# Optimization experiments

Measured on AMD Instinct MI355X. Metric: run time of the kernel, lower is better.

Reference implementation:

```python
import jax, jax.numpy as jnp
import numpy as np

STRIDES = (8, 16, 32)
IMG = 640
REG_MAX = 16
TOPK = 10
ALPHA = 0.5
BETA = 6.0
EPS_IOU = 1e-16


def _make_anchors():
    # anchor centers for all pyramid levels, (N, 2) in pixel coords
    pts = []
    for s in STRIDES:
        h = w = IMG // s
        ys, xs = jnp.meshgrid(jnp.arange(h, dtype=jnp.float32),
                              jnp.arange(w, dtype=jnp.float32), indexing='ij')
        a = (jnp.stack([xs, ys], axis=-1).reshape(-1, 2) + 0.5) * s
        pts.append(a)
    return jnp.concatenate(pts, axis=0)  # (8400, 2)


def _iou_pairwise(pred, gt):
    # pred (B,N,4), gt (B,M,4) -> IoU (B,M,N)
    b1 = pred[:, None, :, :]   # (B,1,N,4)
    b2 = gt[:, :, None, :]     # (B,M,1,4)
    tl = jnp.maximum(b1[..., :2], b2[..., :2])
    br = jnp.minimum(b1[..., 2:], b2[..., 2:])
    wh = jnp.clip(br - tl, 0.0)
    inter = wh[..., 0] * wh[..., 1]
    a1 = (b1[..., 2] - b1[..., 0]) * (b1[..., 3] - b1[..., 1])
    a2 = (b2[..., 2] - b2[..., 0]) * (b2[..., 3] - b2[..., 1])
    return inter / (a1 + a2 - inter + EPS_IOU)


def _iou_1v1(b1, b2):
    # elementwise IoU, both (..., 4)
    tl = jnp.maximum(b1[..., :2], b2[..., :2])
    br = jnp.minimum(b1[..., 2:], b2[..., 2:])
    wh = jnp.clip(br - tl, 0.0)
    inter = wh[..., 0] * wh[..., 1]
    a1 = (b1[..., 2] - b1[..., 0]) * (b1[..., 3] - b1[..., 1])
    a2 = (b2[..., 2] - b2[..., 0]) * (b2[..., 3] - b2[..., 1])
    return inter / (a1 + a2 - inter + EPS_IOU)


def setup_inputs() -> dict:
    key = jax.random.key(0)
    ks = jax.random.split(key, 6)
    B, N, NC, M = 32, 8400, 80, 40
    pred_scores = jax.random.normal(ks[0], (B, N, NC), jnp.float32)
    pred_dist = jax.random.normal(ks[1], (B, N, 4 * REG_MAX), jnp.float32)
    gt_labels = jax.random.randint(ks[2], (B, M, 1), 0, NC, dtype=jnp.int32)
    cxy = jax.random.uniform(ks[3], (B, M, 2), jnp.float32) * 560.0 + 40.0
    wh = jax.random.uniform(ks[4], (B, M, 2), jnp.float32) * 120.0 + 20.0
    gt_bboxes = jnp.concatenate([jnp.clip(cxy - wh / 2, 0.0, float(IMG)),
                                 jnp.clip(cxy + wh / 2, 0.0, float(IMG))], axis=-1)
    dfl_weight = jax.random.normal(ks[5], (REG_MAX,), jnp.float32) * 0.05
    return {"pred_scores": pred_scores, "pred_dist": pred_dist,
            "gt_labels": gt_labels, "gt_bboxes": gt_bboxes,
            "dfl_weight": dfl_weight}


def reference(pred_scores, pred_dist, gt_labels, gt_bboxes, dfl_weight):
    B, N, NC = pred_scores.shape
    M = gt_bboxes.shape[1]
    anchors = _make_anchors()  # (N, 2)

    # DFL: softmax over reg bins, weighted sum with (random-init) conv weight
    prob = jax.nn.softmax(pred_dist.reshape(B, N, 4, REG_MAX), axis=-1)
    ltrb = prob @ dfl_weight                      # (B,N,4)
    pred_bboxes = jnp.concatenate([anchors - ltrb[..., :2],
                                   anchors + ltrb[..., 2:]], axis=-1)  # (B,N,4) xyxy

    # ---- task-aligned assigner (no-grad) ----
    sg = jax.lax.stop_gradient
    sig = jax.nn.sigmoid(sg(pred_scores))         # (B,N,NC)
    labels = gt_labels[..., 0].astype(jnp.int32)  # (B,M)
    sigT = jnp.swapaxes(sig, 1, 2)                # (B,NC,N)
    scores = jnp.take_along_axis(sigT, jnp.broadcast_to(labels[:, :, None], (B, M, N)), axis=1)  # (B,M,N)
    ious = jnp.clip(_iou_pairwise(sg(pred_bboxes), gt_bboxes), 0.0)      # (B,M,N)
    align = scores ** ALPHA * ious ** BETA        # (B,M,N)

    _, topk_idxs = jax.lax.top_k(align, TOPK)     # (B,M,TOPK) over anchors
    mask = jnp.zeros((B * M, N), dtype=align.dtype)
    mask = mask.at[jnp.arange(B * M)[:, None], topk_idxs.reshape(B * M, TOPK)].set(1.0)
    mask = mask.reshape(B, M, N)
    mask = mask * (align > 1e-9).astype(align.dtype)
    max_m = align.max(axis=1)                     # (B,N) best metric per anchor
    mask = mask * (align == max_m[:, None, :]).astype(align.dtype)

    fg_mask = mask.max(axis=1)                    # (B,N) in {0,1}
    tgt_idx = mask.argmax(axis=1)                 # (B,N) assigned gt index
    ts_sum = jnp.maximum(fg_mask.sum(), 1.0)

    # ---- classification targets (vectorized scatter) ----
    asg_labels = jnp.take_along_axis(labels, tgt_idx, axis=1)  # (B,N)
    target_scores = jax.nn.one_hot(asg_labels, NC, dtype=pred_scores.dtype) * (max_m * fg_mask)[..., None]

    x = pred_scores
    bce = jnp.maximum(x, 0.0) - x * target_scores + jnp.log1p(jnp.exp(-jnp.abs(x)))
    loss_cls = bce.sum() / ts_sum

    # ---- box IoU loss on positives (vectorized gather + mask) ----
    gt_asg = jnp.take_along_axis(gt_bboxes, tgt_idx[..., None], axis=1)  # (B,N,4)
    iou1 = _iou_1v1(pred_bboxes, gt_asg)          # (B,N)
    fg = fg_mask.sum()
    loss_box = jnp.where(fg > 0, ((1.0 - iou1) * fg_mask).sum() / fg, 0.0)

    return loss_cls + loss_box * 1.5
```

## Files before the change

### kernel.cpp

```cpp
#include <hip/hip_runtime.h>
#include <cstdint>
#include <cstddef>

#define BB 32
#define NN 8400
#define NCC 80
#define MM 40
#define RM 16
#define TOPKK 10
#define CAP 2048
#define SLOTP 41
#define AB 64

__device__ __forceinline__ void anchor_xy(int n, float& ax, float& ay) {
    int s, x, y;
    if (n < 6400)      { s = 8;  y = n / 80;            x = n - y * 80; }
    else if (n < 8000) { int i = n - 6400; s = 16; y = i / 40; x = i - y * 40; }
    else               { int i = n - 8000; s = 32; y = i / 20; x = i - y * 20; }
    ax = ((float)x + 0.5f) * (float)s;
    ay = ((float)y + 0.5f) * (float)s;
}

__global__ __launch_bounds__(256) void k_dfl(const float* __restrict__ pd,
                                             const float* __restrict__ w,
                                             float* __restrict__ pbb,
                                             int*   __restrict__ tgt) {
    const int b  = blockIdx.y;
    const int n0 = blockIdx.x * 128;
    const int t  = threadIdx.x;

    if (t < 128 && n0 + t < NN) tgt[(size_t)b * NN + n0 + t] = 0x7F7F7F7F;

    #pragma unroll
    for (int h = 0; h < 2; h++) {
        int f = t + h * 256;
        int a = f >> 2, side = f & 3;
        int n = n0 + a;
        int nc = min(n, NN - 1);
        const float* p = pd + (((size_t)(b * NN + nc)) * 4 + side) * RM;
        float x[RM];
        #pragma unroll
        for (int i = 0; i < 4; i++) {
            float4 v = *(const float4*)(p + i * 4);
            x[i*4+0] = v.x; x[i*4+1] = v.y; x[i*4+2] = v.z; x[i*4+3] = v.w;
        }
        float mx = x[0];
        #pragma unroll
        for (int i = 1; i < RM; i++) mx = fmaxf(mx, x[i]);
        float s = 0.f, d = 0.f;
        #pragma unroll
        for (int i = 0; i < RM; i++) {
            float e = __builtin_amdgcn_exp2f((x[i] - mx) * 1.44269504f);
            s += e; d += e * w[i];
        }
        d *= __builtin_amdgcn_rcpf(s);
        float ax, ay; anchor_xy(nc, ax, ay);
        float axy = (side & 1) ? ay : ax;
        float v = (side < 2) ? (axy - d) : (axy + d);
        if (n < NN) pbb[((size_t)(b * NN + n)) * 4 + side] = v;
    }
}

__global__ __launch_bounds__(256) void k_align(const float* __restrict__ ps,
                                               const int*   __restrict__ gl,
                                               const float* __restrict__ gb,
                                               const float* __restrict__ pbb,
                                               float* __restrict__ maxm,
                                               int*   __restrict__ cnts,
                                               unsigned long long* __restrict__ lists,
                                               float* __restrict__ accum) {
    __shared__ float  sc[AB * SLOTP];
    __shared__ float4 box[AB];
    __shared__ float  gtb[MM * 4];
    __shared__ int    glab[MM];
    __shared__ int    slotm[MM];
    __shared__ int    cmap[NCC];
    __shared__ float  cm[256];
    __shared__ float  redf[4];
    const int b  = blockIdx.y;
    const int n0 = blockIdx.x * AB;
    const int t  = threadIdx.x;

    if (t < MM * 4)              gtb[t] = gb[b * MM * 4 + t];
    if (t >= 192 && t < 192+MM)  glab[t - 192] = gl[b * MM + (t - 192)];
    if (t >= 96 && t < 96+NCC)   cmap[t - 96] = 0x7FFFFFFF;
    if (t < AB) {
        int nc = min(n0 + t, NN - 1);
        box[t] = *(const float4*)(pbb + ((size_t)(b * NN + nc)) * 4);
    }
    __syncthreads();
    if (t < MM) atomicMin(&cmap[glab[t]], t);
    __syncthreads();
    if (t < MM) slotm[t] = cmap[glab[t]];

    float4 vv[5];
    #pragma unroll
    for (int k = 0; k < 5; k++) {
        int f = t + k * 256;
        int row = f / 20, c4 = f - row * 20;
        int nc = min(n0 + row, NN - 1);
        vv[k] = *(const float4*)(ps + ((size_t)(b * NN + nc)) * NCC + c4 * 4);
    }
    float sp = 0.f;
    #pragma unroll
    for (int k = 0; k < 5; k++) {
        int f = t + k * 256;
        int row = f / 20, c4 = f - row * 20;
        float vmask = (n0 + row < NN) ? 1.f : 0.f;
        float xs[4] = {vv[k].x, vv[k].y, vv[k].z, vv[k].w};
        #pragma unroll
        for (int j = 0; j < 4; j++) {
            float x = xs[j];
            float e = __builtin_amdgcn_exp2f(-1.44269504f * fabsf(x));
            float r = __builtin_amdgcn_rcpf(1.0f + e);
            sp += vmask * (fmaxf(x, 0.f) + 0.69314718f * __builtin_amdgcn_logf(1.0f + e));
            int sl = cmap[c4 * 4 + j];
            if (sl < MM) sc[row * SLOTP + sl] = (x >= 0.f) ? r : e * r;
        }
    }
    __syncthreads();

    const int nloc = t & 63;
    const int n    = n0 + nloc;
    const int mb   = (t >> 6) * 10;
    const int lane = t & 63;
    const bool valid = (n < NN);
    float cmax = -INFINITY;
    float4 p4 = box[nloc];
    const float px1 = p4.x, py1 = p4.y, px2 = p4.z, py2 = p4.w;
    const float a1 = (px2 - px1) * (py2 - py1);
    #pragma unroll
    for (int j = 0; j < 10; j++) {
        int m = mb + j;
        float gx1 = gtb[m*4+0], gy1 = gtb[m*4+1], gx2 = gtb[m*4+2], gy2 = gtb[m*4+3];
        float a2 = (gx2 - gx1) * (gy2 - gy1);
        float iw = fmaxf(fminf(px2, gx2) - fmaxf(px1, gx1), 0.f);
        float ih = fmaxf(fminf(py2, gy2) - fmaxf(py1, gy1), 0.f);
        float inter = iw * ih;
        float iou = fmaxf(inter * __builtin_amdgcn_rcpf(a1 + a2 - inter + 1e-16f), 0.f);
        float al = 0.f;
        if (valid) {
            float sg = sc[nloc * SLOTP + slotm[m]];
            float i2 = iou * iou;
            al = __builtin_amdgcn_sqrtf(sg) * (i2 * i2 * i2);
        }
        cmax = fmaxf(cmax, al);
        bool pos = valid && (al > 1e-9f);
        unsigned long long msk = __ballot(pos);
        if (msk) {
            int leader = __ffsll((long long)msk) - 1;
            int basev = 0;
            if (lane == leader) basev = atomicAdd(&cnts[b * MM + m], __popcll(msk));
            basev = __shfl(basev, leader);
            if (pos) {
                int ofs = __popcll(msk & ((1ull << lane) - 1ull));
                int idx = basev + ofs;
                if (idx < CAP)
                    lists[((size_t)(b * MM + m)) * CAP + idx] =
                        ((unsigned long long)__float_as_uint(al) << 32) | (unsigned)n;
            }
        }
    }
    cm[t] = cmax;
    __syncthreads();
    if (t < AB && valid)
        maxm[(size_t)b * NN + n] =
            fmaxf(fmaxf(cm[t], cm[t + 64]), fmaxf(cm[t + 128], cm[t + 192]));

    #pragma unroll
    for (int off = 32; off > 0; off >>= 1) sp += __shfl_down(sp, off);
    if ((t & 63) == 0) redf[t >> 6] = sp;
    __syncthreads();
    if (t == 0) atomicAdd(accum, redf[0] + redf[1] + redf[2] + redf[3]);
}

__global__ __launch_bounds__(64) void k_topk(const unsigned long long* __restrict__ lists,
                                             const int*   __restrict__ cnts,
                                             const float* __restrict__ maxm,
                                             int* __restrict__ tgt) {
    __shared__ unsigned long long keys[CAP];
    __shared__ unsigned long long sel[TOPKK];
    const int bm = blockIdx.x, b = bm / MM, m = bm % MM, t = threadIdx.x;
    int cnt = min(cnts[bm], CAP);
    int kk = min(TOPKK, cnt);
    for (int i = t; i < cnt; i += 64) {
        unsigned long long L = lists[(size_t)bm * CAP + i];
        keys[i] = (L & 0xFFFFFFFF00000000ull) | (0xFFFFFFFFull - (L & 0xFFFFFFFFull));
    }
    __syncthreads();
    for (int p = 0; p < kk; p++) {
        unsigned long long best = 0ull;
        for (int i = t; i < cnt; i += 64) best = keys[i] > best ? keys[i] : best;
        #pragma unroll
        for (int off = 32; off > 0; off >>= 1) {
            unsigned long long o = __shfl_xor(best, off);
            best = o > best ? o : best;
        }
        for (int i = t; i < cnt; i += 64) if (keys[i] == best) keys[i] = 0ull;
        if (t == 0) sel[p] = best;
        __syncthreads();
    }
    if (t < kk) {
        unsigned long long bb = sel[t];
        float v = __uint_as_float((unsigned)(bb >> 32));
        int n = (int)(0xFFFFFFFFull - (bb & 0xFFFFFFFFull));
        if (v == maxm[(size_t)b * NN + n]) atomicMin(&tgt[(size_t)b * NN + n], m);
    }
}

__global__ __launch_bounds__(256) void k_fg(const int*   __restrict__ tgt,
                                            const int*   __restrict__ gl,
                                            const float* __restrict__ gb,
                                            const float* __restrict__ ps,
                                            const float* __restrict__ pbb,
                                            const float* __restrict__ maxm,
                                            float* __restrict__ accum) {
    int i = blockIdx.x * 256 + threadIdx.x;
    int t = threadIdx.x;
    float vdot = 0.f, vbox = 0.f, vfg = 0.f;
    int tg = tgt[i];
    if (tg < MM) {
        int b = i / NN;
        int lab = gl[b * MM + tg];
        float x = ps[(size_t)i * NCC + lab];
        float mm = maxm[i];
        float4 p = *(const float4*)(pbb + (size_t)i * 4);
        const float* g = gb + ((size_t)b * MM + tg) * 4;
        float a1 = (p.z - p.x) * (p.w - p.y);
        float a2 = (g[2] - g[0]) * (g[3] - g[1]);
        float iw = fmaxf(fminf(p.z, g[2]) - fmaxf(p.x, g[0]), 0.f);
        float ih = fmaxf(fminf(p.w, g[3]) - fmaxf(p.y, g[1]), 0.f);
        float inter = iw * ih;
        float iou = inter / (a1 + a2 - inter + 1e-16f);
        vdot = x * mm; vbox = 1.0f - iou; vfg = 1.0f;
    }
    #pragma unroll
    for (int off = 32; off > 0; off >>= 1) {
        vdot += __shfl_down(vdot, off);
        vbox += __shfl_down(vbox, off);
        vfg  += __shfl_down(vfg,  off);
    }
    __shared__ float r[3][4];
    if ((t & 63) == 0) { int wv = t >> 6; r[0][wv] = vdot; r[1][wv] = vbox; r[2][wv] = vfg; }
    __syncthreads();
    if (t < 3) {
        float s = r[t][0] + r[t][1] + r[t][2] + r[t][3];
        if (s != 0.f) atomicAdd(&accum[1 + t], s);
    }
}

__global__ void k_final(const float* __restrict__ accum, float* __restrict__ out) {
    float S0 = accum[0], dot = accum[1], box = accum[2], fg = accum[3];
    float ts = fmaxf(fg, 1.0f);
    float cls = (S0 - dot) / ts;
    float lb = (fg > 0.f) ? box / fg : 0.f;
    out[0] = cls + 1.5f * lb;
}

extern "C" void kernel_launch(void* const* d_in, const int* in_sizes, int n_in,
                              void* d_out, int out_size, void* d_ws, size_t ws_size,
                              hipStream_t stream) {
    const float* ps = (const float*)d_in[0];
    const float* pd = (const float*)d_in[1];
    const int*   gl = (const int*)  d_in[2];
    const float* gb = (const float*)d_in[3];
    const float* w  = (const float*)d_in[4];

    char* ws = (char*)d_ws;
    constexpr size_t ACC_BYTES  = 256;
    constexpr size_t CNT_BYTES  = 8192;
    constexpr size_t PBB_BYTES  = (size_t)BB * NN * 4 * sizeof(float);
    constexpr size_t MAXM_BYTES = (size_t)BB * NN * sizeof(float);
    constexpr size_t TGT_BYTES  = (size_t)BB * NN * sizeof(int);

    float* accum = (float*)ws;
    int*   cnts  = (int*)  (ws + ACC_BYTES);
    float* pbb   = (float*)(ws + ACC_BYTES + CNT_BYTES);
    float* maxm  = (float*)(ws + ACC_BYTES + CNT_BYTES + PBB_BYTES);
    int*   tgt   = (int*)  (ws + ACC_BYTES + CNT_BYTES + PBB_BYTES + MAXM_BYTES);
    unsigned long long* lists =
        (unsigned long long*)(ws + ACC_BYTES + CNT_BYTES + PBB_BYTES + MAXM_BYTES + TGT_BYTES);

    hipMemsetAsync(ws, 0, ACC_BYTES + CNT_BYTES, stream);

    dim3 gdfl((NN + 127) / 128, BB);
    k_dfl<<<gdfl, 256, 0, stream>>>(pd, w, pbb, tgt);
    dim3 gal((NN + AB - 1) / AB, BB);
    k_align<<<gal, 256, 0, stream>>>(ps, gl, gb, pbb, maxm, cnts, lists, accum);
    k_topk<<<BB * MM, 64, 0, stream>>>(lists, cnts, maxm, tgt);
    k_fg<<<BB * NN / 256, 256, 0, stream>>>(tgt, gl, gb, ps, pbb, maxm, accum);
    k_final<<<1, 1, 0, stream>>>(accum, (float*)d_out);
}
```

Measured before the change: 224.8 us.

## Fuse DFL box decoding into alignment kernel and add occupancy hint

Merges the DFL decode kernel into the alignment kernel. Each block decodes the boxes for its 64 anchors straight into shared memory, so the decoded boxes no longer have to be read back from global memory and one launch is removed. The pred_dist and score loads are issued up front so they overlap the gt setup. It also raises the launch bounds to ask for 8 blocks per CU, which may cost registers or cause spills.

Result: faster. 218.7 us (-2.7%).

```diff
diff --git a/kernel.cpp b/kernel.cpp
--- a/kernel.cpp
+++ b/kernel.cpp
@@ -21,56 +21,19 @@
     ay = ((float)y + 0.5f) * (float)s;
 }
 
-__global__ __launch_bounds__(256) void k_dfl(const float* __restrict__ pd,
-                                             const float* __restrict__ w,
-                                             float* __restrict__ pbb,
-                                             int*   __restrict__ tgt) {
-    const int b  = blockIdx.y;
-    const int n0 = blockIdx.x * 128;
-    const int t  = threadIdx.x;
-
-    if (t < 128 && n0 + t < NN) tgt[(size_t)b * NN + n0 + t] = 0x7F7F7F7F;
-
-    #pragma unroll
-    for (int h = 0; h < 2; h++) {
-        int f = t + h * 256;
-        int a = f >> 2, side = f & 3;
-        int n = n0 + a;
-        int nc = min(n, NN - 1);
-        const float* p = pd + (((size_t)(b * NN + nc)) * 4 + side) * RM;
-        float x[RM];
-        #pragma unroll
-        for (int i = 0; i < 4; i++) {
-            float4 v = *(const float4*)(p + i * 4);
-            x[i*4+0] = v.x; x[i*4+1] = v.y; x[i*4+2] = v.z; x[i*4+3] = v.w;
-        }
-        float mx = x[0];
-        #pragma unroll
-        for (int i = 1; i < RM; i++) mx = fmaxf(mx, x[i]);
-        float s = 0.f, d = 0.f;
-        #pragma unroll
-        for (int i = 0; i < RM; i++) {
-            float e = __builtin_amdgcn_exp2f((x[i] - mx) * 1.44269504f);
-            s += e; d += e * w[i];
-        }
-        d *= __builtin_amdgcn_rcpf(s);
-        float ax, ay; anchor_xy(nc, ax, ay);
-        float axy = (side & 1) ? ay : ax;
-        float v = (side < 2) ? (axy - d) : (axy + d);
-        if (n < NN) pbb[((size_t)(b * NN + n)) * 4 + side] = v;
-    }
-}
-
-__global__ __launch_bounds__(256) void k_align(const float* __restrict__ ps,
-                                               const int*   __restrict__ gl,
-                                               const float* __restrict__ gb,
-                                               const float* __restrict__ pbb,
-                                               float* __restrict__ maxm,
-                                               int*   __restrict__ cnts,
-                                               unsigned long long* __restrict__ lists,
-                                               float* __restrict__ accum) {
+__global__ __launch_bounds__(256, 8) void k_mono(const float* __restrict__ ps,
+                                                 const float* __restrict__ pd,
+                                                 const int*   __restrict__ gl,
+                                                 const float* __restrict__ gb,
+                                                 const float* __restrict__ w,
+                                                 float* __restrict__ pbb,
+                                                 float* __restrict__ maxm,
+                                                 int*   __restrict__ cnts,
+                                                 unsigned long long* __restrict__ lists,
+                                                 float* __restrict__ accum,
+                                                 int*   __restrict__ tgt) {
     __shared__ float  sc[AB * SLOTP];
-    __shared__ float4 box[AB];
+    __shared__ float  boxf[AB * 4];
     __shared__ float  gtb[MM * 4];
     __shared__ int    glab[MM];
     __shared__ int    slotm[MM];
@@ -81,17 +44,16 @@
     const int n0 = blockIdx.x * AB;
     const int t  = threadIdx.x;
 
-    if (t < MM * 4)              gtb[t] = gb[b * MM * 4 + t];
-    if (t >= 192 && t < 192+MM)  glab[t - 192] = gl[b * MM + (t - 192)];
-    if (t >= 96 && t < 96+NCC)   cmap[t - 96] = 0x7FFFFFFF;
-    if (t < AB) {
-        int nc = min(n0 + t, NN - 1);
-        box[t] = *(const float4*)(pbb + ((size_t)(b * NN + nc)) * 4);
-    }
-    __syncthreads();
-    if (t < MM) atomicMin(&cmap[glab[t]], t);
-    __syncthreads();
-    if (t < MM) slotm[t] = cmap[glab[t]];
+    if (t < AB && n0 + t < NN) tgt[(size_t)b * NN + n0 + t] = 0x7F7F7F7F;
+
+    const int a    = t >> 2, side = t & 3;
+    const int nA   = n0 + a;
+    const int ncA  = min(nA, NN - 1);
+    const float* p = pd + (((size_t)(b * NN + ncA)) * 4 + side) * RM;
+    float4 xa0 = *(const float4*)(p);
+    float4 xa1 = *(const float4*)(p + 4);
+    float4 xa2 = *(const float4*)(p + 8);
+    float4 xa3 = *(const float4*)(p + 12);
 
     float4 vv[5];
     #pragma unroll
@@ -101,6 +63,38 @@
         int nc = min(n0 + row, NN - 1);
         vv[k] = *(const float4*)(ps + ((size_t)(b * NN + nc)) * NCC + c4 * 4);
     }
+
+    if (t < MM * 4)              gtb[t] = gb[b * MM * 4 + t];
+    if (t >= 192 && t < 192+MM)  glab[t - 192] = gl[b * MM + (t - 192)];
+    if (t >= 96 && t < 96+NCC)   cmap[t - 96] = 0x7FFFFFFF;
+    __syncthreads();
+    if (t < MM) atomicMin(&cmap[glab[t]], t);
+    __syncthreads();
+    if (t < MM) slotm[t] = cmap[glab[t]];
+
+    {
+        float x[RM];
+        x[0]=xa0.x;  x[1]=xa0.y;  x[2]=xa0.z;  x[3]=xa0.w;
+        x[4]=xa1.x;  x[5]=xa1.y;  x[6]=xa1.z;  x[7]=xa1.w;
+        x[8]=xa2.x;  x[9]=xa2.y;  x[10]=xa2.z; x[11]=xa2.w;
+        x[12]=xa3.x; x[13]=xa3.y; x[14]=xa3.z; x[15]=xa3.w;
+        float mx = x[0];
+        #pragma unroll
+        for (int i = 1; i < RM; i++) mx = fmaxf(mx, x[i]);
+        float s = 0.f, d = 0.f;
+        #pragma unroll
+        for (int i = 0; i < RM; i++) {
+            float e = __builtin_amdgcn_exp2f((x[i] - mx) * 1.44269504f);
+            s += e; d += e * w[i];
+        }
+        d *= __builtin_amdgcn_rcpf(s);
+        float ax, ay; anchor_xy(ncA, ax, ay);
+        float axy = (side & 1) ? ay : ax;
+        float v = (side < 2) ? (axy - d) : (axy + d);
+        boxf[t] = v;
+        if (nA < NN) pbb[((size_t)(b * NN + nA)) * 4 + side] = v;
+    }
+
     float sp = 0.f;
     #pragma unroll
     for (int k = 0; k < 5; k++) {
@@ -126,7 +120,7 @@
     const int lane = t & 63;
     const bool valid = (n < NN);
     float cmax = -INFINITY;
-    float4 p4 = box[nloc];
+    float4 p4 = ((const float4*)boxf)[nloc];
     const float px1 = p4.x, py1 = p4.y, px2 = p4.z, py2 = p4.w;
     const float a1 = (px2 - px1) * (py2 - py1);
     #pragma unroll
@@ -283,10 +277,8 @@
 
     hipMemsetAsync(ws, 0, ACC_BYTES + CNT_BYTES, stream);
 
-    dim3 gdfl((NN + 127) / 128, BB);
-    k_dfl<<<gdfl, 256, 0, stream>>>(pd, w, pbb, tgt);
-    dim3 gal((NN + AB - 1) / AB, BB);
-    k_align<<<gal, 256, 0, stream>>>(ps, gl, gb, pbb, maxm, cnts, lists, accum);
+    dim3 gmono((NN + AB - 1) / AB, BB);
+    k_mono<<<gmono, 256, 0, stream>>>(ps, pd, gl, gb, w, pbb, maxm, cnts, lists, accum, tgt);
     k_topk<<<BB * MM, 64, 0, stream>>>(lists, cnts, maxm, tgt);
     k_fg<<<BB * NN / 256, 256, 0, stream>>>(tgt, gl, gb, ps, pbb, maxm, accum);
     k_final<<<1, 1, 0, stream>>>(accum, (float*)d_out);
```
